# Kernel tuning notes

Measured on AMD Instinct MI355X. Metric: run time of the kernel, lower is better.

The kernel has to match this reference:

```python
import jax, jax.numpy as jnp
import numpy as np
from jax import lax

DIM = 64
D_STATE = 16
D_CONV = 4
EXPAND = 2
D_INNER = EXPAND * DIM  # 128
EPS = 1e-3  # keras LayerNormalization default epsilon


def setup_inputs() -> dict:
    key = jax.random.key(0)
    ks = jax.random.split(key, 9)
    B, H, W, D = 2, 48, 48, 48
    x = jax.random.normal(ks[0], (B, H, W, D, DIM), dtype=jnp.float32)
    # Dense kernels (fan-in scaled), conv kernel is depthwise: [k, 1, d_inner]
    W_in = jax.random.normal(ks[1], (DIM, 2 * D_INNER), jnp.float32) / np.sqrt(DIM)
    conv_w = jax.random.normal(ks[2], (D_CONV, 1, D_INNER), jnp.float32) / np.sqrt(D_CONV)
    conv_b = jnp.zeros((D_INNER,), jnp.float32)
    W_x = jax.random.normal(ks[3], (D_INNER, D_STATE + D_INNER), jnp.float32) / np.sqrt(D_INNER)
    W_dt = jax.random.normal(ks[4], (D_INNER, D_INNER), jnp.float32) / np.sqrt(D_INNER)
    b_dt = jnp.zeros((D_INNER,), jnp.float32)
    W_out = jax.random.normal(ks[5], (D_INNER, DIM), jnp.float32) / np.sqrt(D_INNER)
    gamma = jnp.ones((DIM,), jnp.float32)
    beta = jnp.zeros((DIM,), jnp.float32)
    return {"x": x, "W_in": W_in, "conv_w": conv_w, "conv_b": conv_b,
            "W_x": W_x, "W_dt": W_dt, "b_dt": b_dt, "W_out": W_out,
            "gamma": gamma, "beta": beta}


def _layernorm(z, gamma, beta):
    mu = jnp.mean(z, axis=-1, keepdims=True)
    var = jnp.mean(jnp.square(z - mu), axis=-1, keepdims=True)
    return gamma * (z - mu) * lax.rsqrt(var + EPS) + beta


def reference(x, W_in, conv_w, conv_b, W_x, W_dt, b_dt, W_out, gamma, beta):
    B, H, W, D, C = x.shape
    L = H * W * D
    x_flat = x.reshape(B, L, C)                       # [B, L, C]
    x_and_res = x_flat @ W_in                         # [B, L, 2*d_inner]
    x_ssm, res = jnp.split(x_and_res, 2, axis=-1)     # each [B, L, d_inner]
    # depthwise Conv1D, kernel=4, TF 'same' padding (pad_left=1, pad_right=2)
    x_ssm = lax.conv_general_dilated(
        x_ssm, conv_w, window_strides=(1,), padding=[(1, 2)],
        dimension_numbers=("NWC", "WIO", "NWC"), feature_group_count=D_INNER) + conv_b
    x_ssm = jax.nn.silu(x_ssm)
    # simplified SSM: projections + softplus + cumulative-sum scan over L
    x_proj = x_ssm @ W_x                              # [B, L, d_state+d_inner]
    dt = jax.nn.softplus(x_ssm @ W_dt + b_dt)         # [B, L, d_inner]
    state = jnp.cumsum(x_proj[..., :D_INNER] * dt, axis=1)  # [B, L, d_inner]
    y = state * jax.nn.silu(res)                      # gated output
    out = (y @ W_out).reshape(B, H, W, D, C)
    return _layernorm(out + x, gamma, beta)
```

## Files before the change

kernel.cpp:

```cpp
#include <hip/hip_runtime.h>
#include <hip/hip_bf16.h>
#include <math.h>

#define L_LEN 110592
#define TILE 32
#define NT 3456
#define NCH 64
#define TPC 54
#define XS_S 60

typedef float  floatx4 __attribute__((ext_vector_type(4)));
typedef short  short8  __attribute__((ext_vector_type(8)));
typedef short  short4v __attribute__((ext_vector_type(4)));

__device__ __forceinline__ float fast_silu(float v) {
    return v * __builtin_amdgcn_rcpf(1.f + __expf(-v));
}
__device__ __forceinline__ float fast_softplus(float d) {
    return fmaxf(d, 0.f) + __logf(1.f + __expf(-fabsf(d)));
}
__device__ __forceinline__ short f2bf(float f) {
    __hip_bfloat16 h = __float2bfloat16(f);
    return *reinterpret_cast<short*>(&h);
}
__device__ __forceinline__ float bf2f(short s) {
    __hip_bfloat16 h = *reinterpret_cast<__hip_bfloat16*>(&s);
    return __bfloat162float(h);
}
__device__ __forceinline__ short8 pack_bf8(float4 a, float4 b) {
    short8 r;
    r[0] = f2bf(a.x); r[1] = f2bf(a.y); r[2] = f2bf(a.z); r[3] = f2bf(a.w);
    r[4] = f2bf(b.x); r[5] = f2bf(b.y); r[6] = f2bf(b.z); r[7] = f2bf(b.w);
    return r;
}

__global__ __launch_bounds__(256) void kW_w(
    const float* __restrict__ W_in, const float* __restrict__ W_x,
    const float* __restrict__ W_dt, const float* __restrict__ W_out,
    __hip_bfloat16* __restrict__ wti, __hip_bfloat16* __restrict__ wpt,
    __hip_bfloat16* __restrict__ wtr, __hip_bfloat16* __restrict__ wot)
{
    const int t = threadIdx.x;
    for (int idx = t; idx < 128 * 64; idx += 256) {
        int n = idx >> 6, k = idx & 63;
        wti[idx] = __float2bfloat16(W_in[k * 256 + n]);
        wtr[idx] = __float2bfloat16(W_in[k * 256 + 128 + n]);
    }
    for (int idx = t; idx < 256 * 128; idx += 256) {
        int n = idx >> 7, k = idx & 127;
        float v = (n < 128) ? W_x[k * 144 + n] : W_dt[k * 128 + (n - 128)];
        wpt[idx] = __float2bfloat16(v);
    }
    for (int idx = t; idx < 64 * 128; idx += 256) {
        int n = idx >> 7, k = idx & 127;
        wot[idx] = __float2bfloat16(W_out[k * 64 + n]);
    }
}

__global__ __launch_bounds__(256) void kA(
    const float* __restrict__ x,
    const __hip_bfloat16* __restrict__ wti,
    const __hip_bfloat16* __restrict__ wpt,
    const float* __restrict__ conv_w, const float* __restrict__ conv_b,
    const float* __restrict__ b_dt,
    __hip_bfloat16* __restrict__ s, float* __restrict__ sums)
{
    __shared__ __hip_bfloat16 xs[128 * XS_S];
    __shared__ __hip_bfloat16 xcb[32 * 136];

    const int t = threadIdx.x;
    const int lane = t & 63;
    const int w = t >> 6;
    const int quad = lane >> 4;
    const int lr = lane & 15;
    const int tile = blockIdx.x;
    const int b = blockIdx.y;
    const int l0 = tile * TILE;

    {
        floatx4 acc[3][2] = {};
        #pragma unroll
        for (int ks = 0; ks < 2; ++ks) {
            short8 bfr[2];
            #pragma unroll
            for (int j = 0; j < 2; ++j) {
                const int n = w * 32 + j * 16 + lr;
                bfr[j] = *(const short8*)(wti + (n << 6) + ks * 32 + quad * 8);
            }
            #pragma unroll
            for (int mt = 0; mt < 3; ++mt) {
                const long row = (long)l0 - 1 + mt * 16 + lr;
                const bool ok = (row >= 0) && (row < L_LEN);
                const float* xp = x + (((long)b * L_LEN + (ok ? row : 0)) << 6)
                                    + ks * 32 + quad * 8;
                float4 u0 = {0.f,0.f,0.f,0.f}, u1 = {0.f,0.f,0.f,0.f};
                if (ok) { u0 = ((const float4*)xp)[0]; u1 = ((const float4*)xp)[1]; }
                short8 afr = pack_bf8(u0, u1);
                acc[mt][0] = __builtin_amdgcn_mfma_f32_16x16x32_bf16(afr, bfr[0], acc[mt][0], 0, 0, 0);
                acc[mt][1] = __builtin_amdgcn_mfma_f32_16x16x32_bf16(afr, bfr[1], acc[mt][1], 0, 0, 0);
            }
        }
        #pragma unroll
        for (int mt = 0; mt < 3; ++mt)
            #pragma unroll
            for (int j = 0; j < 2; ++j) {
                const int col = w * 32 + j * 16 + lr;
                short4v pk;
                pk.x = f2bf(acc[mt][j][0]); pk.y = f2bf(acc[mt][j][1]);
                pk.z = f2bf(acc[mt][j][2]); pk.w = f2bf(acc[mt][j][3]);
                *(short4v*)&xs[col * XS_S + mt * 16 + quad * 4] = pk;
            }
    }
    __syncthreads();

    {
        const int c = t & 127;
        const int m0 = (t >> 7) * 16;
        const float cw0 = conv_w[c], cw1 = conv_w[128 + c];
        const float cw2 = conv_w[256 + c], cw3 = conv_w[384 + c];
        const float cb = conv_b[c];
        float wb[20];
        #pragma unroll
        for (int j = 0; j < 5; ++j) {
            short4v sv = *(const short4v*)&xs[c * XS_S + m0 + j * 4];
            wb[j*4+0] = bf2f(sv.x); wb[j*4+1] = bf2f(sv.y);
            wb[j*4+2] = bf2f(sv.z); wb[j*4+3] = bf2f(sv.w);
        }
        #pragma unroll
        for (int i = 0; i < 16; ++i) {
            float v = wb[i] * cw0 + wb[i + 1] * cw1 + wb[i + 2] * cw2
                    + wb[i + 3] * cw3 + cb;
            xcb[(m0 + i) * 136 + c] = __float2bfloat16(fast_silu(v));
        }
    }
    __syncthreads();

    {
        floatx4 accx[2][2] = {}, accd[2][2] = {};
        #pragma unroll
        for (int ks = 0; ks < 4; ++ks) {
            short8 afr[2];
            #pragma unroll
            for (int mt = 0; mt < 2; ++mt)
                afr[mt] = *(const short8*)&xcb[(mt * 16 + lr) * 136 + ks * 32 + quad * 8];
            #pragma unroll
            for (int j = 0; j < 2; ++j) {
                const int n = w * 32 + j * 16 + lr;
                short8 bx = *(const short8*)(wpt + (n << 7) + ks * 32 + quad * 8);
                short8 bd = *(const short8*)(wpt + ((n + 128) << 7) + ks * 32 + quad * 8);
                #pragma unroll
                for (int mt = 0; mt < 2; ++mt) {
                    accx[mt][j] = __builtin_amdgcn_mfma_f32_16x16x32_bf16(afr[mt], bx, accx[mt][j], 0, 0, 0);
                    accd[mt][j] = __builtin_amdgcn_mfma_f32_16x16x32_bf16(afr[mt], bd, accd[mt][j], 0, 0, 0);
                }
            }
        }
        const long base = (long)b * L_LEN + l0;
        float ps0 = 0.f, ps1 = 0.f;
        #pragma unroll
        for (int j = 0; j < 2; ++j) {
            const int col = w * 32 + j * 16 + lr;
            const float bdv = b_dt[col];
            float psl = 0.f;
            #pragma unroll
            for (int mt = 0; mt < 2; ++mt) {
                #pragma unroll
                for (int r = 0; r < 4; ++r) {
                    float dv = accd[mt][j][r] + bdv;
                    float sv = accx[mt][j][r] * fast_softplus(dv);
                    __hip_bfloat16 h = __float2bfloat16(sv);
                    s[((base + mt * 16 + quad * 4 + r) << 7) + col] = h;
                    psl += __bfloat162float(h);
                }
            }
            if (j == 0) ps0 = psl; else ps1 = psl;
        }
        ps0 += __shfl_xor(ps0, 16); ps0 += __shfl_xor(ps0, 32);
        ps1 += __shfl_xor(ps1, 16); ps1 += __shfl_xor(ps1, 32);
        const long sb = ((long)b * NT + tile) << 7;
        if (quad == 0)      sums[sb + w * 32 + lr] = ps0;
        else if (quad == 1) sums[sb + w * 32 + 16 + lr] = ps1;
    }
}

__global__ __launch_bounds__(256) void kB1(const float* __restrict__ sums,
                                           float* __restrict__ csum)
{
    __shared__ float ps[256];
    const int t = threadIdx.x;
    const int c = t & 127, h = t >> 7;
    const int ch = blockIdx.x, b = blockIdx.y;
    const long tb = ((long)b * NT + ch * TPC + h * 27) * 128 + c;
    float tot = 0.f;
    for (int j = 0; j < 27; j += 9) {
        float v[9];
        #pragma unroll
        for (int k = 0; k < 9; ++k) v[k] = sums[tb + (long)(j + k) * 128];
        #pragma unroll
        for (int k = 0; k < 9; ++k) tot += v[k];
    }
    ps[t] = tot;
    __syncthreads();
    if (t < 128) csum[((long)b * NCH + ch) * 128 + t] = ps[t] + ps[t + 128];
}

__global__ __launch_bounds__(256) void kB2(float* __restrict__ csum)
{
    const int t = threadIdx.x;
    const int c = t & 127, b = t >> 7;
    const long base = (long)b * NCH * 128 + c;
    float run = 0.f;
    for (int ch = 0; ch < NCH; ch += 8) {
        float v[8];
        #pragma unroll
        for (int k = 0; k < 8; ++k) v[k] = csum[base + (long)(ch + k) * 128];
        #pragma unroll
        for (int k = 0; k < 8; ++k) {
            csum[base + (long)(ch + k) * 128] = run;
            run += v[k];
        }
    }
}

__global__ __launch_bounds__(128) void kB3(float* __restrict__ sums,
                                           const float* __restrict__ csum)
{
    const int c = threadIdx.x;
    const int ch = blockIdx.x, b = blockIdx.y;
    float run = csum[((long)b * NCH + ch) * 128 + c];
    const long tb = ((long)b * NT + ch * TPC) * 128 + c;
    for (int j = 0; j < TPC; j += 9) {
        float v[9];
        #pragma unroll
        for (int k = 0; k < 9; ++k) v[k] = sums[tb + (long)(j + k) * 128];
        #pragma unroll
        for (int k = 0; k < 9; ++k) {
            sums[tb + (long)(j + k) * 128] = run;
            run += v[k];
        }
    }
}

__global__ __launch_bounds__(256) void kC(
    const float* __restrict__ x,
    const __hip_bfloat16* __restrict__ wtr,
    const __hip_bfloat16* __restrict__ wot,
    const float* __restrict__ gamma, const float* __restrict__ beta,
    const __hip_bfloat16* __restrict__ s, const float* __restrict__ offs,
    float* __restrict__ out)
{
    __shared__ float resf[32 * 128];
    __shared__ __hip_bfloat16 ybf[32 * 136];

    const int t = threadIdx.x;
    const int lane = t & 63;
    const int w = t >> 6;
    const int quad = lane >> 4;
    const int lr = lane & 15;
    const int tile = blockIdx.x;
    const int b = blockIdx.y;
    const int l0 = tile * TILE;
    const long base = (long)b * L_LEN;

    {
        floatx4 acc[2][2] = {};
        #pragma unroll
        for (int ks = 0; ks < 2; ++ks) {
            short8 bfr[2];
            #pragma unroll
            for (int j = 0; j < 2; ++j) {
                const int n = w * 32 + j * 16 + lr;
                bfr[j] = *(const short8*)(wtr + (n << 6) + ks * 32 + quad * 8);
            }
            #pragma unroll
            for (int mt = 0; mt < 2; ++mt) {
                const float* xp = x + ((base + l0 + mt * 16 + lr) << 6) + ks * 32 + quad * 8;
                float4 u0 = ((const float4*)xp)[0], u1 = ((const float4*)xp)[1];
                short8 afr = pack_bf8(u0, u1);
                acc[mt][0] = __builtin_amdgcn_mfma_f32_16x16x32_bf16(afr, bfr[0], acc[mt][0], 0, 0, 0);
                acc[mt][1] = __builtin_amdgcn_mfma_f32_16x16x32_bf16(afr, bfr[1], acc[mt][1], 0, 0, 0);
            }
        }
        #pragma unroll
        for (int mt = 0; mt < 2; ++mt)
            #pragma unroll
            for (int j = 0; j < 2; ++j) {
                const int col = w * 32 + j * 16 + lr;
                #pragma unroll
                for (int r = 0; r < 4; ++r)
                    resf[(mt * 16 + quad * 4 + r) * 128 + col] = fast_silu(acc[mt][j][r]);
            }
    }
    __syncthreads();

    if (t < 128) {
        float run = offs[((long)b * NT + tile) * 128 + t];
        const __hip_bfloat16* sp = s + ((base + l0) << 7) + t;
        #pragma unroll 8
        for (int q = 0; q < 32; ++q) {
            run += __bfloat162float(sp[q << 7]);
            ybf[q * 136 + t] = __float2bfloat16(resf[q * 128 + t] * run);
        }
    }
    __syncthreads();

    {
        float* zbuf = resf;
        floatx4 acc[2] = {};
        const int n = w * 16 + lr;
        #pragma unroll
        for (int ks = 0; ks < 4; ++ks) {
            short8 bfr = *(const short8*)(wot + (n << 7) + ks * 32 + quad * 8);
            #pragma unroll
            for (int mt = 0; mt < 2; ++mt) {
                short8 afr = *(const short8*)&ybf[(mt * 16 + lr) * 136 + ks * 32 + quad * 8];
                acc[mt] = __builtin_amdgcn_mfma_f32_16x16x32_bf16(afr, bfr, acc[mt], 0, 0, 0);
            }
        }
        __syncthreads();
        #pragma unroll
        for (int mt = 0; mt < 2; ++mt)
            #pragma unroll
            for (int r = 0; r < 4; ++r)
                zbuf[(mt * 16 + quad * 4 + r) * 68 + n] = acc[mt][r];
    }
    __syncthreads();

    {
        const float* zbuf = resf;
        const int d = t & 63;
        const int dg = t >> 6;
        const float g  = gamma[d];
        const float bt = beta[d];
        #pragma unroll 2
        for (int i = 0; i < 8; ++i) {
            int q = dg + 4 * i;
            float z = zbuf[q * 68 + d] + x[(base + l0 + q) * 64 + d];
            float zsum = z;
            #pragma unroll
            for (int off = 32; off > 0; off >>= 1) zsum += __shfl_xor(zsum, off);
            float mu = zsum * 0.015625f;
            float dz = z - mu;
            float vsum = dz * dz;
            #pragma unroll
            for (int off = 32; off > 0; off >>= 1) vsum += __shfl_xor(vsum, off);
            float inv = rsqrtf(vsum * 0.015625f + 1e-3f);
            out[(base + l0 + q) * 64 + d] = g * dz * inv + bt;
        }
    }
}

extern "C" void kernel_launch(void* const* d_in, const int* in_sizes, int n_in,
                              void* d_out, int out_size, void* d_ws, size_t ws_size,
                              hipStream_t stream) {
    const float* x      = (const float*)d_in[0];
    const float* W_in   = (const float*)d_in[1];
    const float* conv_w = (const float*)d_in[2];
    const float* conv_b = (const float*)d_in[3];
    const float* W_x    = (const float*)d_in[4];
    const float* W_dt   = (const float*)d_in[5];
    const float* b_dt   = (const float*)d_in[6];
    const float* W_out  = (const float*)d_in[7];
    const float* gamma  = (const float*)d_in[8];
    const float* beta   = (const float*)d_in[9];
    float* out = (float*)d_out;

    __hip_bfloat16* s    = (__hip_bfloat16*)d_ws;
    float*          sums = (float*)((char*)d_ws + 56623104);
    float*          csum = (float*)((char*)d_ws + 60162048);
    __hip_bfloat16* wti  = (__hip_bfloat16*)((char*)d_ws + 88477696);
    __hip_bfloat16* wpt  = (__hip_bfloat16*)((char*)d_ws + 88494080);
    __hip_bfloat16* wtr  = (__hip_bfloat16*)((char*)d_ws + 88559616);
    __hip_bfloat16* wot  = (__hip_bfloat16*)((char*)d_ws + 88576000);

    kW_w<<<1, 256, 0, stream>>>(W_in, W_x, W_dt, W_out, wti, wpt, wtr, wot);
    dim3 grid(NT, 2);
    kA<<<grid, 256, 0, stream>>>(x, wti, wpt, conv_w, conv_b, b_dt, s, sums);
    dim3 gridB(NCH, 2);
    kB1<<<gridB, 256, 0, stream>>>(sums, csum);
    kB2<<<1, 256, 0, stream>>>(csum);
    kB3<<<gridB, 128, 0, stream>>>(sums, csum);
    kC<<<grid, 256, 0, stream>>>(x, wtr, wot, gamma, beta, s, sums, out);
}
```

Before: 318.5 us.

## Transpose scan buffer to channel-major, stage x in LDS, fuse conv into registers

The intermediate s buffer becomes channel-major ([B,128,L]), so kA writes packed 4-element stores and kC reads 16 contiguous bf16 per thread and does a two-half parallel prefix instead of a 32-step serial scan on half the threads. x tiles are staged once into LDS as bf16 in both kernels, and the depthwise conv is computed from MFMA accumulators using cross-lane shuffles, which drops the xs transpose buffer and one barrier. Occupancy hints are added to the launch bounds and LDS strides are changed. The changes target uncoalesced 2-byte scatter stores and the serial scan, at the cost of a strided layout for other consumers of s and extra register pressure.

```diff
diff --git a/kernel.cpp b/kernel.cpp
--- a/kernel.cpp
+++ b/kernel.cpp
@@ -7,7 +7,9 @@
 #define NT 3456
 #define NCH 64
 #define TPC 54
-#define XS_S 60
+#define STRX 72
+#define STRC 136
+#define RESS 132
 
 typedef float  floatx4 __attribute__((ext_vector_type(4)));
 typedef short  short8  __attribute__((ext_vector_type(8)));
@@ -57,7 +59,7 @@
     }
 }
 
-__global__ __launch_bounds__(256) void kA(
+__global__ __launch_bounds__(256, 8) void kA(
     const float* __restrict__ x,
     const __hip_bfloat16* __restrict__ wti,
     const __hip_bfloat16* __restrict__ wpt,
@@ -65,8 +67,8 @@
     const float* __restrict__ b_dt,
     __hip_bfloat16* __restrict__ s, float* __restrict__ sums)
 {
-    __shared__ __hip_bfloat16 xs[128 * XS_S];
-    __shared__ __hip_bfloat16 xcb[32 * 136];
+    __shared__ __align__(16) __hip_bfloat16 xbf[48 * STRX];
+    __shared__ __align__(16) __hip_bfloat16 xcb[32 * STRC];
 
     const int t = threadIdx.x;
     const int lane = t & 63;
@@ -77,60 +79,59 @@
     const int b = blockIdx.y;
     const int l0 = tile * TILE;
 
+    for (int idx = t; idx < 384; idx += 256) {
+        const int row = idx >> 3, c8 = (idx & 7) << 3;
+        const long gr = (long)l0 - 1 + row;
+        float4 u0 = {0.f, 0.f, 0.f, 0.f}, u1 = {0.f, 0.f, 0.f, 0.f};
+        if (gr >= 0 && gr < L_LEN) {
+            const float* xp = x + (((long)b * L_LEN + gr) << 6) + c8;
+            u0 = ((const float4*)xp)[0];
+            u1 = ((const float4*)xp)[1];
+        }
+        *(short8*)&xbf[row * STRX + c8] = pack_bf8(u0, u1);
+    }
+    __syncthreads();
+
     {
         floatx4 acc[3][2] = {};
         #pragma unroll
         for (int ks = 0; ks < 2; ++ks) {
-            short8 bfr[2];
-            #pragma unroll
-            for (int j = 0; j < 2; ++j) {
-                const int n = w * 32 + j * 16 + lr;
-                bfr[j] = *(const short8*)(wti + (n << 6) + ks * 32 + quad * 8);
-            }
+            short8 bfr0 = *(const short8*)(wti + ((w * 32 + lr) << 6) + ks * 32 + quad * 8);
+            short8 bfr1 = *(const short8*)(wti + ((w * 32 + 16 + lr) << 6) + ks * 32 + quad * 8);
             #pragma unroll
             for (int mt = 0; mt < 3; ++mt) {
-                const long row = (long)l0 - 1 + mt * 16 + lr;
-                const bool ok = (row >= 0) && (row < L_LEN);
-                const float* xp = x + (((long)b * L_LEN + (ok ? row : 0)) << 6)
-                                    + ks * 32 + quad * 8;
-                float4 u0 = {0.f,0.f,0.f,0.f}, u1 = {0.f,0.f,0.f,0.f};
-                if (ok) { u0 = ((const float4*)xp)[0]; u1 = ((const float4*)xp)[1]; }
-                short8 afr = pack_bf8(u0, u1);
-                acc[mt][0] = __builtin_amdgcn_mfma_f32_16x16x32_bf16(afr, bfr[0], acc[mt][0], 0, 0, 0);
-                acc[mt][1] = __builtin_amdgcn_mfma_f32_16x16x32_bf16(afr, bfr[1], acc[mt][1], 0, 0, 0);
-            }
-        }
-        #pragma unroll
-        for (int mt = 0; mt < 3; ++mt)
-            #pragma unroll
-            for (int j = 0; j < 2; ++j) {
-                const int col = w * 32 + j * 16 + lr;
-                short4v pk;
-                pk.x = f2bf(acc[mt][j][0]); pk.y = f2bf(acc[mt][j][1]);
-                pk.z = f2bf(acc[mt][j][2]); pk.w = f2bf(acc[mt][j][3]);
-                *(short4v*)&xs[col * XS_S + mt * 16 + quad * 4] = pk;
-            }
-    }
-    __syncthreads();
-
-    {
-        const int c = t & 127;
-        const int m0 = (t >> 7) * 16;
-        const float cw0 = conv_w[c], cw1 = conv_w[128 + c];
-        const float cw2 = conv_w[256 + c], cw3 = conv_w[384 + c];
-        const float cb = conv_b[c];
-        float wb[20];
-        #pragma unroll
-        for (int j = 0; j < 5; ++j) {
-            short4v sv = *(const short4v*)&xs[c * XS_S + m0 + j * 4];
-            wb[j*4+0] = bf2f(sv.x); wb[j*4+1] = bf2f(sv.y);
-            wb[j*4+2] = bf2f(sv.z); wb[j*4+3] = bf2f(sv.w);
-        }
-        #pragma unroll
-        for (int i = 0; i < 16; ++i) {
-            float v = wb[i] * cw0 + wb[i + 1] * cw1 + wb[i + 2] * cw2
-                    + wb[i + 3] * cw3 + cb;
-            xcb[(m0 + i) * 136 + c] = __float2bfloat16(fast_silu(v));
+                short8 afr = *(const short8*)&xbf[(mt * 16 + lr) * STRX + ks * 32 + quad * 8];
+                acc[mt][0] = __builtin_amdgcn_mfma_f32_16x16x32_bf16(afr, bfr0, acc[mt][0], 0, 0, 0);
+                acc[mt][1] = __builtin_amdgcn_mfma_f32_16x16x32_bf16(afr, bfr1, acc[mt][1], 0, 0, 0);
+            }
+        }
+        const int srcLane = (((quad + 1) & 3) << 4) | lr;
+        #pragma unroll
+        for (int jj = 0; jj < 2; ++jj) {
+            const int col = w * 32 + jj * 16 + lr;
+            const float cw0 = conv_w[col],       cw1 = conv_w[128 + col];
+            const float cw2 = conv_w[256 + col], cw3 = conv_w[384 + col];
+            const float cb = conv_b[col];
+            #pragma unroll
+            for (int m = 0; m < 2; ++m) {
+                float s0 = (quad == 0) ? acc[m + 1][jj][0] : acc[m][jj][0];
+                float s1 = (quad == 0) ? acc[m + 1][jj][1] : acc[m][jj][1];
+                float s2 = (quad == 0) ? acc[m + 1][jj][2] : acc[m][jj][2];
+                const float e0 = __shfl(s0, srcLane);
+                const float e1 = __shfl(s1, srcLane);
+                const float e2 = __shfl(s2, srcLane);
+                const float a0 = acc[m][jj][0], a1 = acc[m][jj][1];
+                const float a2 = acc[m][jj][2], a3 = acc[m][jj][3];
+                const int rb = m * 16 + quad * 4;
+                xcb[(rb + 0) * STRC + col] =
+                    __float2bfloat16(fast_silu(cb + cw0 * a0 + cw1 * a1 + cw2 * a2 + cw3 * a3));
+                xcb[(rb + 1) * STRC + col] =
+                    __float2bfloat16(fast_silu(cb + cw0 * a1 + cw1 * a2 + cw2 * a3 + cw3 * e0));
+                xcb[(rb + 2) * STRC + col] =
+                    __float2bfloat16(fast_silu(cb + cw0 * a2 + cw1 * a3 + cw2 * e0 + cw3 * e1));
+                xcb[(rb + 3) * STRC + col] =
+                    __float2bfloat16(fast_silu(cb + cw0 * a3 + cw1 * e0 + cw2 * e1 + cw3 * e2));
+            }
         }
     }
     __syncthreads();
@@ -142,7 +143,7 @@
             short8 afr[2];
             #pragma unroll
             for (int mt = 0; mt < 2; ++mt)
-                afr[mt] = *(const short8*)&xcb[(mt * 16 + lr) * 136 + ks * 32 + quad * 8];
+                afr[mt] = *(const short8*)&xcb[(mt * 16 + lr) * STRC + ks * 32 + quad * 8];
             #pragma unroll
             for (int j = 0; j < 2; ++j) {
                 const int n = w * 32 + j * 16 + lr;
@@ -155,23 +156,25 @@
                 }
             }
         }
-        const long base = (long)b * L_LEN + l0;
         float ps0 = 0.f, ps1 = 0.f;
         #pragma unroll
         for (int j = 0; j < 2; ++j) {
             const int col = w * 32 + j * 16 + lr;
             const float bdv = b_dt[col];
+            __hip_bfloat16* sp = s + ((long)b * 128 + col) * L_LEN + l0 + quad * 4;
             float psl = 0.f;
             #pragma unroll
             for (int mt = 0; mt < 2; ++mt) {
+                short4v pk;
                 #pragma unroll
                 for (int r = 0; r < 4; ++r) {
                     float dv = accd[mt][j][r] + bdv;
                     float sv = accx[mt][j][r] * fast_softplus(dv);
-                    __hip_bfloat16 h = __float2bfloat16(sv);
-                    s[((base + mt * 16 + quad * 4 + r) << 7) + col] = h;
-                    psl += __bfloat162float(h);
+                    short h = f2bf(sv);
+                    pk[r] = h;
+                    psl += bf2f(h);
                 }
+                *(short4v*)(sp + mt * 16) = pk;
             }
             if (j == 0) ps0 = psl; else ps1 = psl;
         }
@@ -241,7 +244,7 @@
     }
 }
 
-__global__ __launch_bounds__(256) void kC(
+__global__ __launch_bounds__(256, 6) void kC(
     const float* __restrict__ x,
     const __hip_bfloat16* __restrict__ wtr,
     const __hip_bfloat16* __restrict__ wot,
@@ -249,8 +252,12 @@
     const __hip_bfloat16* __restrict__ s, const float* __restrict__ offs,
     float* __restrict__ out)
 {
-    __shared__ float resf[32 * 128];
-    __shared__ __hip_bfloat16 ybf[32 * 136];
+    __shared__ float resf[32 * RESS];
+    __shared__ __align__(16) char ubuf[32 * STRC * 2];
+    __shared__ float totbuf[256];
+
+    __hip_bfloat16* const ybf = (__hip_bfloat16*)ubuf;
+    __hip_bfloat16* const xbf = (__hip_bfloat16*)ubuf;
 
     const int t = threadIdx.x;
     const int lane = t & 63;
@@ -263,22 +270,24 @@
     const long base = (long)b * L_LEN;
 
     {
+        const int row = t >> 3, c8 = (t & 7) << 3;
+        const float* xp = x + ((base + l0 + row) << 6) + c8;
+        float4 u0 = ((const float4*)xp)[0], u1 = ((const float4*)xp)[1];
+        *(short8*)&xbf[row * STRX + c8] = pack_bf8(u0, u1);
+    }
+    __syncthreads();
+
+    {
         floatx4 acc[2][2] = {};
         #pragma unroll
         for (int ks = 0; ks < 2; ++ks) {
-            short8 bfr[2];
-            #pragma unroll
-            for (int j = 0; j < 2; ++j) {
-                const int n = w * 32 + j * 16 + lr;
-                bfr[j] = *(const short8*)(wtr + (n << 6) + ks * 32 + quad * 8);
-            }
+            short8 bfr0 = *(const short8*)(wtr + ((w * 32 + lr) << 6) + ks * 32 + quad * 8);
+            short8 bfr1 = *(const short8*)(wtr + ((w * 32 + 16 + lr) << 6) + ks * 32 + quad * 8);
             #pragma unroll
             for (int mt = 0; mt < 2; ++mt) {
-                const float* xp = x + ((base + l0 + mt * 16 + lr) << 6) + ks * 32 + quad * 8;
-                float4 u0 = ((const float4*)xp)[0], u1 = ((const float4*)xp)[1];
-                short8 afr = pack_bf8(u0, u1);
-                acc[mt][0] = __builtin_amdgcn_mfma_f32_16x16x32_bf16(afr, bfr[0], acc[mt][0], 0, 0, 0);
-                acc[mt][1] = __builtin_amdgcn_mfma_f32_16x16x32_bf16(afr, bfr[1], acc[mt][1], 0, 0, 0);
+                short8 afr = *(const short8*)&xbf[(mt * 16 + lr) * STRX + ks * 32 + quad * 8];
+                acc[mt][0] = __builtin_amdgcn_mfma_f32_16x16x32_bf16(afr, bfr0, acc[mt][0], 0, 0, 0);
+                acc[mt][1] = __builtin_amdgcn_mfma_f32_16x16x32_bf16(afr, bfr1, acc[mt][1], 0, 0, 0);
             }
         }
         #pragma unroll
@@ -288,19 +297,30 @@
                 const int col = w * 32 + j * 16 + lr;
                 #pragma unroll
                 for (int r = 0; r < 4; ++r)
-                    resf[(mt * 16 + quad * 4 + r) * 128 + col] = fast_silu(acc[mt][j][r]);
-            }
-    }
-    __syncthreads();
-
-    if (t < 128) {
-        float run = offs[((long)b * NT + tile) * 128 + t];
-        const __hip_bfloat16* sp = s + ((base + l0) << 7) + t;
-        #pragma unroll 8
-        for (int q = 0; q < 32; ++q) {
-            run += __bfloat162float(sp[q << 7]);
-            ybf[q * 136 + t] = __float2bfloat16(resf[q * 128 + t] * run);
-        }
+                    resf[(mt * 16 + quad * 4 + r) * RESS + col] = fast_silu(acc[mt][j][r]);
+            }
+    }
+    __syncthreads();
+
+    {
+        const int c = t & 127, h = t >> 7;
+        const __hip_bfloat16* sp = s + ((long)b * 128 + c) * L_LEN + l0 + h * 16;
+        short8 sv0 = *(const short8*)sp;
+        short8 sv1 = *(const short8*)(sp + 8);
+        float pfx[16];
+        float run = 0.f;
+        #pragma unroll
+        for (int i = 0; i < 8; ++i) { run += bf2f(sv0[i]); pfx[i] = run; }
+        #pragma unroll
+        for (int i = 0; i < 8; ++i) { run += bf2f(sv1[i]); pfx[8 + i] = run; }
+        totbuf[t] = run;
+        __syncthreads();
+        float off = offs[((long)b * NT + tile) * 128 + c];
+        if (h) off += totbuf[c];
+        #pragma unroll
+        for (int q = 0; q < 16; ++q)
+            ybf[(h * 16 + q) * STRC + c] =
+                __float2bfloat16(resf[(h * 16 + q) * RESS + c] * (off + pfx[q]));
     }
     __syncthreads();
 
@@ -313,11 +333,10 @@
             short8 bfr = *(const short8*)(wot + (n << 7) + ks * 32 + quad * 8);
             #pragma unroll
             for (int mt = 0; mt < 2; ++mt) {
-                short8 afr = *(const short8*)&ybf[(mt * 16 + lr) * 136 + ks * 32 + quad * 8];
+                short8 afr = *(const short8*)&ybf[(mt * 16 + lr) * STRC + ks * 32 + quad * 8];
                 acc[mt] = __builtin_amdgcn_mfma_f32_16x16x32_bf16(afr, bfr, acc[mt], 0, 0, 0);
             }
         }
-        __syncthreads();
         #pragma unroll
         for (int mt = 0; mt < 2; ++mt)
             #pragma unroll
```

After: 325.9 us. +2.3%, slower.
